# Kernel tuning notes

Measured on AMD Instinct MI355X. Metric: run time of the kernel, lower is better.

Reference implementation:

```python
import jax, jax.numpy as jnp
import numpy as np

N_NODES = 100000
N_EDGES = 1600000
IN_DIM, HIDDEN_DIM, OUT_DIM = 500, 64, 40


def setup_inputs() -> dict:
    key = jax.random.key(0)
    k1, k2, k3, k4, k5 = jax.random.split(key, 5)
    x = jax.random.normal(k1, (N_NODES, IN_DIM), dtype=jnp.float32)
    edge_index = jax.random.randint(k2, (2, N_EDGES), 0, N_NODES, dtype=jnp.int64)
    # Glorot-style init like PyG GCNConv
    W1 = jax.random.normal(k3, (IN_DIM, HIDDEN_DIM), dtype=jnp.float32) / np.sqrt(IN_DIM)
    b1 = jnp.zeros((HIDDEN_DIM,), dtype=jnp.float32)
    W2 = jax.random.normal(k4, (HIDDEN_DIM, OUT_DIM), dtype=jnp.float32) / np.sqrt(HIDDEN_DIM)
    b2 = jnp.zeros((OUT_DIM,), dtype=jnp.float32)
    return {"x": x, "W1": W1, "b1": b1, "W2": W2, "b2": b2, "edge_index": edge_index}


def _gcn_conv(x, W, b, src, dst, n):
    """PyG GCNConv: h = D^{-1/2} (A + I) D^{-1/2} (x W) + b."""
    h = x @ W  # transform first, propagate in smaller dim
    loops = jnp.arange(n, dtype=src.dtype)
    s = jnp.concatenate([src, loops])
    d = jnp.concatenate([dst, loops])
    deg = jax.ops.segment_sum(jnp.ones_like(d, dtype=h.dtype), d, num_segments=n)
    dinv = jnp.where(deg > 0, jax.lax.rsqrt(deg), 0.0)
    norm = dinv[s] * dinv[d]               # [E+N]
    msg = h[s] * norm[:, None]             # gather + scale
    out = jax.ops.segment_sum(msg, d, num_segments=n)  # scatter-add
    return out + b


def reference(x, W1, b1, W2, b2, edge_index):
    src, dst = edge_index[0], edge_index[1]
    n = x.shape[0]
    h = _gcn_conv(x, W1, b1, src, dst, n)
    h = jax.nn.relu(h)  # eval mode: dropout is identity
    out = _gcn_conv(h, W2, b2, src, dst, n)
    return out
```

## Files before the change

### kernel.cpp

```cpp
#include <hip/hip_runtime.h>
#include <cstdint>
#include <cstddef>

#define NN 100000
#define NE 1600000
#define IND 500
#define HD 64
#define OD 40
#define NBLK ((NN + 255) / 256)
#define KSTEPS 16
#define NTT 16
#define EB 1563

typedef __attribute__((ext_vector_type(8))) short short8v;
typedef __attribute__((ext_vector_type(8))) __bf16 bf16x8;
typedef __attribute__((ext_vector_type(4))) float float4v;

template <class V>
static __device__ __forceinline__ auto mfma_bf16_(V a, V b, float4v c, int)
    -> decltype(__builtin_amdgcn_mfma_f32_16x16x32_bf16(a, b, c, 0, 0, 0)) {
    return __builtin_amdgcn_mfma_f32_16x16x32_bf16(a, b, c, 0, 0, 0);
}
template <class V>
static __device__ __forceinline__ float4v mfma_bf16_(V a, V b, float4v c, long) {
    return __builtin_amdgcn_mfma_f32_16x16x32_bf16((bf16x8)a, (bf16x8)b, c, 0, 0, 0);
}
static __device__ __forceinline__ float4v mfma16(short8v a, short8v b, float4v c) {
    return mfma_bf16_(a, b, c, 0);
}

static __device__ __forceinline__ float bf2f(unsigned short v) {
    return __uint_as_float((unsigned)v << 16);
}
static __device__ __forceinline__ unsigned short f2bf(float v) {
    unsigned u = __float_as_uint(v);
    return (unsigned short)((u + 0x7fffu + ((u >> 16) & 1u)) >> 16);
}

typedef __attribute__((address_space(3))) char lds_char;
typedef const __attribute__((address_space(1))) char g_char;
static __device__ __forceinline__ void gl16(const char* g, char* l) {
    __builtin_amdgcn_global_load_lds((g_char*)g, (lds_char*)l, 16, 0, 0);
}

static __device__ __forceinline__ int detect64(const void* ei) {
    const unsigned* u = (const unsigned*)ei;
    int is64 = 1;
    #pragma unroll
    for (int i = 1; i < 16; i += 2)
        if (u[i] != 0u) is64 = 0;
    return is64;
}

static __device__ __forceinline__ void load4e(const void* ei, int is64, size_t base, int v[4]) {
    if (is64) {
        int4 a = ((const int4*)ei)[base >> 1];
        int4 b = ((const int4*)ei)[(base >> 1) + 1];
        v[0] = a.x; v[1] = a.z; v[2] = b.x; v[3] = b.z;
    } else {
        int4 a = *(const int4*)((const int*)ei + base);
        v[0] = a.x; v[1] = a.y; v[2] = a.z; v[3] = a.w;
    }
}

__global__ __launch_bounds__(256) void k_count_prep(const void* ei, int* cnt,
                                                    int* __restrict__ rank,
                                                    const float* __restrict__ W,
                                                    unsigned short* __restrict__ wh,
                                                    unsigned short* __restrict__ wl) {
    const int is64 = detect64(ei);
    int e0 = (blockIdx.x * 256 + threadIdx.x) * 4;
    if (e0 < NE) {
        int d[4];
        load4e(ei, is64, (size_t)NE + e0, d);
        int4 r;
        r.x = atomicAdd(&cnt[d[0]], 1);
        r.y = atomicAdd(&cnt[d[1]], 1);
        r.z = atomicAdd(&cnt[d[2]], 1);
        r.w = atomicAdd(&cnt[d[3]], 1);
        *(int4*)(rank + e0) = r;
    }
    int t = blockIdx.x * 256 + threadIdx.x;
    if (t < KSTEPS * 4 * 64) {
        int l = t & 63;
        int f = (t >> 6) & 3;
        int s = t >> 8;
        int n = f * 16 + (l & 15);
        int kbase = s * 32 + 8 * (l >> 4);
        unsigned short* ph = wh + (size_t)t * 8;
        unsigned short* pl = wl + (size_t)t * 8;
        #pragma unroll
        for (int j = 0; j < 8; ++j) {
            int k = kbase + j;
            float v = (k < IND) ? W[(size_t)k * HD + n] : 0.f;
            unsigned u = __float_as_uint(v);
            ph[j] = (unsigned short)(u >> 16);
            float r = v - __uint_as_float(u & 0xffff0000u);
            pl[j] = f2bf(r);
        }
    }
}

__global__ __launch_bounds__(256) void k_scan_block(const int* __restrict__ cnt,
                                                    int* __restrict__ rowptr,
                                                    int* __restrict__ bsum,
                                                    float* __restrict__ dinv) {
    int t = threadIdx.x;
    int i = blockIdx.x * 256 + t;
    int v = (i < NN) ? cnt[i] : 0;
    if (i < NN) dinv[i] = rsqrtf((float)v + 1.0f);
    int inc = v;
    #pragma unroll
    for (int off = 1; off < 64; off <<= 1) {
        int u = __shfl_up(inc, off);
        if ((t & 63) >= off) inc += u;
    }
    __shared__ int wsum[4];
    if ((t & 63) == 63) wsum[t >> 6] = inc;
    __syncthreads();
    if (t == 0) {
        int a = 0;
        #pragma unroll
        for (int w = 0; w < 4; ++w) { int b = wsum[w]; wsum[w] = a; a += b; }
        bsum[blockIdx.x] = a;
    }
    __syncthreads();
    if (i < NN) rowptr[i] = inc - v + wsum[t >> 6];
}

__global__ __launch_bounds__(512) void k_scan_bsum(int* bsum) {
    int t = threadIdx.x;
    int v = (t < NBLK) ? bsum[t] : 0;
    int inc = v;
    #pragma unroll
    for (int off = 1; off < 64; off <<= 1) {
        int u = __shfl_up(inc, off);
        if ((t & 63) >= off) inc += u;
    }
    __shared__ int wsum[8];
    if ((t & 63) == 63) wsum[t >> 6] = inc;
    __syncthreads();
    if (t == 0) {
        int a = 0;
        #pragma unroll
        for (int w = 0; w < 8; ++w) { int b = wsum[w]; wsum[w] = a; a += b; }
    }
    __syncthreads();
    if (t < NBLK) bsum[t] = inc - v + wsum[t >> 6];
}

__global__ void k_scan_add(int* rowptr, const int* __restrict__ bsum) {
    int i = blockIdx.x * 256 + threadIdx.x;
    if (i < NN) rowptr[i] += bsum[i >> 8];
    if (i == 0) rowptr[NN] = NE;
}

__global__ void k_scatter(const void* ei, const int* __restrict__ rowptr,
                          const int* __restrict__ rank, int* __restrict__ srcs) {
    int e0 = (blockIdx.x * 256 + threadIdx.x) * 4;
    if (e0 >= NE) return;
    const int is64 = detect64(ei);
    int s[4], d[4];
    load4e(ei, is64, (size_t)e0, s);
    load4e(ei, is64, (size_t)NE + e0, d);
    int4 r = *(const int4*)(rank + e0);
    srcs[rowptr[d[0]] + r.x] = s[0];
    srcs[rowptr[d[1]] + r.y] = s[1];
    srcs[rowptr[d[2]] + r.z] = s[2];
    srcs[rowptr[d[3]] + r.w] = s[3];
}

static __device__ __forceinline__ void split8f(float4 u0, float4 u1,
                                               short8v& hi, short8v& lo) {
    float t[8] = {u0.x, u0.y, u0.z, u0.w, u1.x, u1.y, u1.z, u1.w};
    #pragma unroll
    for (int j = 0; j < 8; ++j) {
        unsigned q = __float_as_uint(t[j]);
        hi[j] = (short)(q >> 16);
        float r = t[j] - __uint_as_float(q & 0xffff0000u);
        lo[j] = (short)f2bf(r);
    }
}

__global__ __launch_bounds__(256, 5) void k_gemm1m(const float* __restrict__ x,
                                                   const char* __restrict__ whb,
                                                   const char* __restrict__ wlb,
                                                   const float* __restrict__ dinv,
                                                   unsigned short* __restrict__ h) {
    __shared__ char smem[32768];
    const int tid  = threadIdx.x;
    const int lane = tid & 63;
    const int wave = tid >> 6;
    const int row0 = blockIdx.x * 64;
    const int rA = lane & 15;
    const int cg = lane >> 4;

    auto stage = [&](int kt, int buf) {
        const bool tail = (kt == NTT - 1);
        #pragma unroll
        for (int i = 0; i < 2; ++i) {
            int slot = i * 256 + tid;
            int r = slot >> 3, c = slot & 7;
            int cs = c ^ (r & 7);
            if (tail && cs > 4) cs = 4;
            int rsrc = row0 + r; if (rsrc >= NN) rsrc = NN - 1;
            const char* g = (const char*)x + (size_t)rsrc * (IND * 4) + kt * 128 + cs * 16;
            char* l = smem + buf * 16384 + (i * 256 + wave * 64) * 16;
            gl16(g, l);
        }
        #pragma unroll
        for (int i = 0; i < 2; ++i) {
            int j = i * 256 + tid;
            const char* src = (j < 256 ? whb : wlb) + kt * 4096 + (size_t)(j & 255) * 16;
            char* l = smem + buf * 16384 + 8192 + (i * 256 + wave * 64) * 16;
            gl16(src, l);
        }
    };

    float4v acc[4];
    const float4v zero4 = {0.f, 0.f, 0.f, 0.f};
    #pragma unroll
    for (int f = 0; f < 4; ++f) acc[f] = zero4;

    stage(0, 0);
    stage(1, 1);

    const int rbase = (wave * 16 + rA) * 8;
    const int sw = rA & 7;

    for (int kt = 0; kt < NTT; ++kt) {
        if (kt + 1 < NTT) asm volatile("s_waitcnt vmcnt(4)\ns_barrier" ::: "memory");
        else              asm volatile("s_waitcnt vmcnt(0)\ns_barrier" ::: "memory");
        const float4*  pa = (const float4*)(smem + (kt & 1) * 16384);
        const short8v* pb = (const short8v*)(smem + (kt & 1) * 16384 + 8192);
        int ch = cg * 2;
        float4 u0 = pa[rbase + (ch ^ sw)];
        float4 u1 = pa[rbase + ((ch + 1) ^ sw)];
        short8v ah, al;
        split8f(u0, u1, ah, al);
        #pragma unroll
        for (int f = 0; f < 4; ++f) {
            short8v vh = pb[f * 64 + lane];
            short8v vl = pb[256 + f * 64 + lane];
            acc[f] = mfma16(al, vh, acc[f]);
            acc[f] = mfma16(ah, vl, acc[f]);
            acc[f] = mfma16(ah, vh, acc[f]);
        }
        if (kt + 2 < NTT) {
            asm volatile("s_barrier" ::: "memory");
            stage(kt + 2, kt & 1);
        }
    }

    #pragma unroll
    for (int j = 0; j < 4; ++j) {
        int row = row0 + wave * 16 + cg * 4 + j;
        if (row < NN) {
            float dv = dinv[row];
            #pragma unroll
            for (int f = 0; f < 4; ++f)
                h[(size_t)row * HD + f * 16 + rA] = f2bf(acc[f][j] * dv);
        }
    }
}

__global__ __launch_bounds__(256) void k_agg1(const int* __restrict__ rowptr,
                                              const int* __restrict__ srcs,
                                              const float* __restrict__ dinv,
                                              const unsigned short* __restrict__ hb,
                                              const float* __restrict__ bias,
                                              unsigned short* __restrict__ outb) {
    int wid = (blockIdx.x * 256 + threadIdx.x) >> 6;
    int lane = threadIdx.x & 63;
    if (wid >= NN) return;
    float acc = bf2f(hb[(size_t)wid * HD + lane]);
    int beg = rowptr[wid];
    int cnt = rowptr[wid + 1] - beg;
    for (int base = 0; base < cnt; base += 64) {
        int m = cnt - base; if (m > 64) m = 64;
        int sj = (lane < m) ? srcs[beg + base + lane] : 0;
        int j = 0;
        for (; j + 8 <= m; j += 8) {
            int s0 = __builtin_amdgcn_readlane(sj, j);
            int s1 = __builtin_amdgcn_readlane(sj, j + 1);
            int s2 = __builtin_amdgcn_readlane(sj, j + 2);
            int s3 = __builtin_amdgcn_readlane(sj, j + 3);
            int s4 = __builtin_amdgcn_readlane(sj, j + 4);
            int s5 = __builtin_amdgcn_readlane(sj, j + 5);
            int s6 = __builtin_amdgcn_readlane(sj, j + 6);
            int s7 = __builtin_amdgcn_readlane(sj, j + 7);
            float v0 = bf2f(hb[(size_t)s0 * HD + lane]);
            float v1 = bf2f(hb[(size_t)s1 * HD + lane]);
            float v2 = bf2f(hb[(size_t)s2 * HD + lane]);
            float v3 = bf2f(hb[(size_t)s3 * HD + lane]);
            float v4 = bf2f(hb[(size_t)s4 * HD + lane]);
            float v5 = bf2f(hb[(size_t)s5 * HD + lane]);
            float v6 = bf2f(hb[(size_t)s6 * HD + lane]);
            float v7 = bf2f(hb[(size_t)s7 * HD + lane]);
            acc += ((v0 + v1) + (v2 + v3)) + ((v4 + v5) + (v6 + v7));
        }
        for (; j < m; ++j) {
            int s = __builtin_amdgcn_readlane(sj, j);
            acc += bf2f(hb[(size_t)s * HD + lane]);
        }
    }
    float dn = dinv[wid];
    outb[(size_t)wid * HD + lane] = f2bf(fmaxf(acc * dn + bias[lane], 0.f) * dn);
}

__global__ __launch_bounds__(256) void k_agg2_gemm2(const int* __restrict__ rowptr,
                                                    const int* __restrict__ srcs,
                                                    const float* __restrict__ dinv,
                                                    const unsigned short* __restrict__ hb,
                                                    const float* __restrict__ W2,
                                                    const float* __restrict__ b2,
                                                    float* __restrict__ out) {
    __shared__ float ws2[HD][OD];
    __shared__ float hsh[4][HD];
    const int t = threadIdx.x;
    for (int i = t; i < HD * OD; i += 256)
        ws2[i / OD][i % OD] = W2[i];

    int wid = (blockIdx.x * 256 + t) >> 6;
    int lane = t & 63;
    int w = t >> 6;
    float acc = bf2f(hb[(size_t)wid * HD + lane]);
    int beg = rowptr[wid];
    int cnt = rowptr[wid + 1] - beg;
    for (int base = 0; base < cnt; base += 64) {
        int m = cnt - base; if (m > 64) m = 64;
        int sj = (lane < m) ? srcs[beg + base + lane] : 0;
        int j = 0;
        for (; j + 8 <= m; j += 8) {
            int s0 = __builtin_amdgcn_readlane(sj, j);
            int s1 = __builtin_amdgcn_readlane(sj, j + 1);
            int s2 = __builtin_amdgcn_readlane(sj, j + 2);
            int s3 = __builtin_amdgcn_readlane(sj, j + 3);
            int s4 = __builtin_amdgcn_readlane(sj, j + 4);
            int s5 = __builtin_amdgcn_readlane(sj, j + 5);
            int s6 = __builtin_amdgcn_readlane(sj, j + 6);
            int s7 = __builtin_amdgcn_readlane(sj, j + 7);
            float v0 = bf2f(hb[(size_t)s0 * HD + lane]);
            float v1 = bf2f(hb[(size_t)s1 * HD + lane]);
            float v2 = bf2f(hb[(size_t)s2 * HD + lane]);
            float v3 = bf2f(hb[(size_t)s3 * HD + lane]);
            float v4 = bf2f(hb[(size_t)s4 * HD + lane]);
            float v5 = bf2f(hb[(size_t)s5 * HD + lane]);
            float v6 = bf2f(hb[(size_t)s6 * HD + lane]);
            float v7 = bf2f(hb[(size_t)s7 * HD + lane]);
            acc += ((v0 + v1) + (v2 + v3)) + ((v4 + v5) + (v6 + v7));
        }
        for (; j < m; ++j) {
            int s = __builtin_amdgcn_readlane(sj, j);
            acc += bf2f(hb[(size_t)s * HD + lane]);
        }
    }
    hsh[w][lane] = acc * dinv[wid];
    __syncthreads();
    if (lane < OD) {
        float s = b2[lane];
        #pragma unroll
        for (int k = 0; k < HD; ++k)
            s = fmaf(hsh[w][k], ws2[k][lane], s);
        out[(size_t)wid * OD + lane] = s;
    }
}

extern "C" void kernel_launch(void* const* d_in, const int* in_sizes, int n_in,
                              void* d_out, int out_size, void* d_ws, size_t ws_size,
                              hipStream_t stream) {
    const float* x  = (const float*)d_in[0];
    const float* W1 = (const float*)d_in[1];
    const float* b1 = (const float*)d_in[2];
    const float* W2 = (const float*)d_in[3];
    const float* b2 = (const float*)d_in[4];
    const void*  ei = d_in[5];
    float* out = (float*)d_out;

    char* ws = (char*)d_ws;
    unsigned short* h1b    = (unsigned short*)ws;
    unsigned short* hrelub = (unsigned short*)(ws + 12800000);
    int*   rowptr = (int*)(ws + 25600000);
    int*   cnt    = (int*)(ws + 26000896);
    int*   bsum   = (int*)(ws + 26401792);
    int*   srcs   = (int*)(ws + 26403840);
    int*   rank   = (int*)(ws + 32803840);
    float* dinv   = (float*)(ws + 39203840);
    unsigned short* wh = (unsigned short*)(ws + 39604224);
    unsigned short* wl = (unsigned short*)(ws + 39669760);

    hipMemsetAsync(cnt, 0, (size_t)NN * 4, stream);
    k_count_prep<<<EB, 256, 0, stream>>>(ei, cnt, rank, W1, wh, wl);
    k_scan_block<<<NBLK, 256, 0, stream>>>(cnt, rowptr, bsum, dinv);
    k_scan_bsum<<<1, 512, 0, stream>>>(bsum);
    k_scan_add<<<NBLK, 256, 0, stream>>>(rowptr, bsum);
    k_scatter<<<EB, 256, 0, stream>>>(ei, rowptr, rank, srcs);
    k_gemm1m<<<EB, 256, 0, stream>>>(x, (const char*)wh, (const char*)wl, dinv, h1b);
    k_agg1<<<(NN * 64) / 256, 256, 0, stream>>>(rowptr, srcs, dinv, h1b, b1, hrelub);
    k_agg2_gemm2<<<(NN * 64) / 256, 256, 0, stream>>>(rowptr, srcs, dinv, hrelub, W2, b2, out);
}
```

Measured before the change: 303.0 us.

## Fuse CSR scatter into GEMM1 kernel and unroll gather loop to 16

The edge scatter that builds the CSR source list is moved into the tail of the first GEMM kernel, which uses the same grid size, so one kernel launch and its dependency gap go away. The scatter's memory traffic can also overlap with GEMM work in other blocks. Separately, the neighbor gather in both aggregation kernels is factored into a helper that issues 16 independent loads per step instead of 8, for more memory-level parallelism. The wider unroll adds register pressure, and the GEMM kernel gains extra tail work.

```diff
diff --git a/kernel.cpp b/kernel.cpp
--- a/kernel.cpp
+++ b/kernel.cpp
@@ -155,21 +155,6 @@
     if (i == 0) rowptr[NN] = NE;
 }
 
-__global__ void k_scatter(const void* ei, const int* __restrict__ rowptr,
-                          const int* __restrict__ rank, int* __restrict__ srcs) {
-    int e0 = (blockIdx.x * 256 + threadIdx.x) * 4;
-    if (e0 >= NE) return;
-    const int is64 = detect64(ei);
-    int s[4], d[4];
-    load4e(ei, is64, (size_t)e0, s);
-    load4e(ei, is64, (size_t)NE + e0, d);
-    int4 r = *(const int4*)(rank + e0);
-    srcs[rowptr[d[0]] + r.x] = s[0];
-    srcs[rowptr[d[1]] + r.y] = s[1];
-    srcs[rowptr[d[2]] + r.z] = s[2];
-    srcs[rowptr[d[3]] + r.w] = s[3];
-}
-
 static __device__ __forceinline__ void split8f(float4 u0, float4 u1,
                                                short8v& hi, short8v& lo) {
     float t[8] = {u0.x, u0.y, u0.z, u0.w, u1.x, u1.y, u1.z, u1.w};
@@ -186,7 +171,11 @@
                                                    const char* __restrict__ whb,
                                                    const char* __restrict__ wlb,
                                                    const float* __restrict__ dinv,
-                                                   unsigned short* __restrict__ h) {
+                                                   unsigned short* __restrict__ h,
+                                                   const void* __restrict__ ei,
+                                                   const int* __restrict__ rowptr,
+                                                   const int* __restrict__ rank,
+                                                   int* __restrict__ srcs) {
     __shared__ char smem[32768];
     const int tid  = threadIdx.x;
     const int lane = tid & 63;
@@ -262,6 +251,60 @@
                 h[(size_t)row * HD + f * 16 + rA] = f2bf(acc[f][j] * dv);
         }
     }
+
+    {
+        int e0 = (blockIdx.x * 256 + tid) * 4;
+        if (e0 < NE) {
+            const int is64 = detect64(ei);
+            int s[4], d[4];
+            load4e(ei, is64, (size_t)e0, s);
+            load4e(ei, is64, (size_t)NE + e0, d);
+            int4 r = *(const int4*)(rank + e0);
+            srcs[rowptr[d[0]] + r.x] = s[0];
+            srcs[rowptr[d[1]] + r.y] = s[1];
+            srcs[rowptr[d[2]] + r.z] = s[2];
+            srcs[rowptr[d[3]] + r.w] = s[3];
+        }
+    }
+}
+
+static __device__ __forceinline__ float csr_gather(const int* __restrict__ rowptr,
+                                                   const int* __restrict__ srcs,
+                                                   const unsigned short* __restrict__ hb,
+                                                   int wid, int lane, float acc) {
+    int beg = rowptr[wid];
+    int cnt = rowptr[wid + 1] - beg;
+    for (int base = 0; base < cnt; base += 64) {
+        int m = cnt - base; if (m > 64) m = 64;
+        int sj = (lane < m) ? srcs[beg + base + lane] : 0;
+        int j = 0;
+        for (; j + 16 <= m; j += 16) {
+            float v[16];
+            #pragma unroll
+            for (int q = 0; q < 16; ++q) {
+                int sq = __builtin_amdgcn_readlane(sj, j + q);
+                v[q] = bf2f(hb[(size_t)sq * HD + lane]);
+            }
+            float t0 = ((v[0] + v[1]) + (v[2] + v[3])) + ((v[4] + v[5]) + (v[6] + v[7]));
+            float t1 = ((v[8] + v[9]) + (v[10] + v[11])) + ((v[12] + v[13]) + (v[14] + v[15]));
+            acc += t0 + t1;
+        }
+        if (j + 8 <= m) {
+            float v[8];
+            #pragma unroll
+            for (int q = 0; q < 8; ++q) {
+                int sq = __builtin_amdgcn_readlane(sj, j + q);
+                v[q] = bf2f(hb[(size_t)sq * HD + lane]);
+            }
+            acc += ((v[0] + v[1]) + (v[2] + v[3])) + ((v[4] + v[5]) + (v[6] + v[7]));
+            j += 8;
+        }
+        for (; j < m; ++j) {
+            int s = __builtin_amdgcn_readlane(sj, j);
+            acc += bf2f(hb[(size_t)s * HD + lane]);
+        }
+    }
+    return acc;
 }
 
 __global__ __launch_bounds__(256) void k_agg1(const int* __restrict__ rowptr,
@@ -274,36 +317,7 @@
     int lane = threadIdx.x & 63;
     if (wid >= NN) return;
     float acc = bf2f(hb[(size_t)wid * HD + lane]);
-    int beg = rowptr[wid];
-    int cnt = rowptr[wid + 1] - beg;
-    for (int base = 0; base < cnt; base += 64) {
-        int m = cnt - base; if (m > 64) m = 64;
-        int sj = (lane < m) ? srcs[beg + base + lane] : 0;
-        int j = 0;
-        for (; j + 8 <= m; j += 8) {
-            int s0 = __builtin_amdgcn_readlane(sj, j);
-            int s1 = __builtin_amdgcn_readlane(sj, j + 1);
-            int s2 = __builtin_amdgcn_readlane(sj, j + 2);
-            int s3 = __builtin_amdgcn_readlane(sj, j + 3);
-            int s4 = __builtin_amdgcn_readlane(sj, j + 4);
-            int s5 = __builtin_amdgcn_readlane(sj, j + 5);
-            int s6 = __builtin_amdgcn_readlane(sj, j + 6);
-            int s7 = __builtin_amdgcn_readlane(sj, j + 7);
-            float v0 = bf2f(hb[(size_t)s0 * HD + lane]);
-            float v1 = bf2f(hb[(size_t)s1 * HD + lane]);
-            float v2 = bf2f(hb[(size_t)s2 * HD + lane]);
-            float v3 = bf2f(hb[(size_t)s3 * HD + lane]);
-            float v4 = bf2f(hb[(size_t)s4 * HD + lane]);
-            float v5 = bf2f(hb[(size_t)s5 * HD + lane]);
-            float v6 = bf2f(hb[(size_t)s6 * HD + lane]);
-            float v7 = bf2f(hb[(size_t)s7 * HD + lane]);
-            acc += ((v0 + v1) + (v2 + v3)) + ((v4 + v5) + (v6 + v7));
-        }
-        for (; j < m; ++j) {
-            int s = __builtin_amdgcn_readlane(sj, j);
-            acc += bf2f(hb[(size_t)s * HD + lane]);
-        }
-    }
+    acc = csr_gather(rowptr, srcs, hb, wid, lane, acc);
     float dn = dinv[wid];
     outb[(size_t)wid * HD + lane] = f2bf(fmaxf(acc * dn + bias[lane], 0.f) * dn);
 }
@@ -325,36 +339,7 @@
     int lane = t & 63;
     int w = t >> 6;
     float acc = bf2f(hb[(size_t)wid * HD + lane]);
-    int beg = rowptr[wid];
-    int cnt = rowptr[wid + 1] - beg;
-    for (int base = 0; base < cnt; base += 64) {
-        int m = cnt - base; if (m > 64) m = 64;
-        int sj = (lane < m) ? srcs[beg + base + lane] : 0;
-        int j = 0;
-        for (; j + 8 <= m; j += 8) {
-            int s0 = __builtin_amdgcn_readlane(sj, j);
-            int s1 = __builtin_amdgcn_readlane(sj, j + 1);
-            int s2 = __builtin_amdgcn_readlane(sj, j + 2);
-            int s3 = __builtin_amdgcn_readlane(sj, j + 3);
-            int s4 = __builtin_amdgcn_readlane(sj, j + 4);
-            int s5 = __builtin_amdgcn_readlane(sj, j + 5);
-            int s6 = __builtin_amdgcn_readlane(sj, j + 6);
-            int s7 = __builtin_amdgcn_readlane(sj, j + 7);
-            float v0 = bf2f(hb[(size_t)s0 * HD + lane]);
-            float v1 = bf2f(hb[(size_t)s1 * HD + lane]);
-            float v2 = bf2f(hb[(size_t)s2 * HD + lane]);
-            float v3 = bf2f(hb[(size_t)s3 * HD + lane]);
-            float v4 = bf2f(hb[(size_t)s4 * HD + lane]);
-            float v5 = bf2f(hb[(size_t)s5 * HD + lane]);
-            float v6 = bf2f(hb[(size_t)s6 * HD + lane]);
-            float v7 = bf2f(hb[(size_t)s7 * HD + lane]);
-            acc += ((v0 + v1) + (v2 + v3)) + ((v4 + v5) + (v6 + v7));
-        }
-        for (; j < m; ++j) {
-            int s = __builtin_amdgcn_readlane(sj, j);
-            acc += bf2f(hb[(size_t)s * HD + lane]);
-        }
-    }
+    acc = csr_gather(rowptr, srcs, hb, wid, lane, acc);
     hsh[w][lane] = acc * dinv[wid];
     __syncthreads();
     if (lane < OD) {
@@ -394,8 +379,8 @@
     k_scan_block<<<NBLK, 256, 0, stream>>>(cnt, rowptr, bsum, dinv);
     k_scan_bsum<<<1, 512, 0, stream>>>(bsum);
     k_scan_add<<<NBLK, 256, 0, stream>>>(rowptr, bsum);
-    k_scatter<<<EB, 256, 0, stream>>>(ei, rowptr, rank, srcs);
-    k_gemm1m<<<EB, 256, 0, stream>>>(x, (const char*)wh, (const char*)wl, dinv, h1b);
+    k_gemm1m<<<EB, 256, 0, stream>>>(x, (const char*)wh, (const char*)wl, dinv, h1b,
+                                     ei, rowptr, rank, srcs);
     k_agg1<<<(NN * 64) / 256, 256, 0, stream>>>(rowptr, srcs, dinv, h1b, b1, hrelub);
     k_agg2_gemm2<<<(NN * 64) / 256, 256, 0, stream>>>(rowptr, srcs, dinv, hrelub, W2, b2, out);
 }
```

Measured after the change: 307.9 us. Within noise of the previous version (+1.6%).

## Project layer-2 features before aggregation using an MFMA projection kernel

Applied to the files above, without the earlier changes.

Reorders the second GCN layer so that the 64-to-40 weight transform runs first in a new MFMA kernel (k_proj), storing the projected features as bf16. Neighbour aggregation then gathers 40-wide rows instead of 64-wide ones. This also removes the per-block shared-memory load of W2 and the scalar per-node GEMM. In exchange there is one extra kernel launch and an extra 8MB write and read of the projected matrix. Lanes 40-63 still issue gathers whose results are thrown away.

```diff
diff --git a/kernel.cpp b/kernel.cpp
--- a/kernel.cpp
+++ b/kernel.cpp
@@ -65,9 +65,12 @@
 
 __global__ __launch_bounds__(256) void k_count_prep(const void* ei, int* cnt,
                                                     int* __restrict__ rank,
-                                                    const float* __restrict__ W,
+                                                    const float* __restrict__ W1,
                                                     unsigned short* __restrict__ wh,
-                                                    unsigned short* __restrict__ wl) {
+                                                    unsigned short* __restrict__ wl,
+                                                    const float* __restrict__ W2,
+                                                    unsigned short* __restrict__ wh2,
+                                                    unsigned short* __restrict__ wl2) {
     const int is64 = detect64(ei);
     int e0 = (blockIdx.x * 256 + threadIdx.x) * 4;
     if (e0 < NE) {
@@ -92,7 +95,26 @@
         #pragma unroll
         for (int j = 0; j < 8; ++j) {
             int k = kbase + j;
-            float v = (k < IND) ? W[(size_t)k * HD + n] : 0.f;
+            float v = (k < IND) ? W1[(size_t)k * HD + n] : 0.f;
+            unsigned u = __float_as_uint(v);
+            ph[j] = (unsigned short)(u >> 16);
+            float r = v - __uint_as_float(u & 0xffff0000u);
+            pl[j] = f2bf(r);
+        }
+    }
+    if (t >= 4096 && t < 4096 + 384) {
+        int t2 = t - 4096;
+        int l = t2 & 63;
+        int f = (t2 >> 6) % 3;
+        int s = t2 / 192;
+        int n = f * 16 + (l & 15);
+        int kbase = s * 32 + 8 * (l >> 4);
+        unsigned short* ph = wh2 + (size_t)t2 * 8;
+        unsigned short* pl = wl2 + (size_t)t2 * 8;
+        #pragma unroll
+        for (int j = 0; j < 8; ++j) {
+            int k = kbase + j;
+            float v = (n < OD) ? W2[(size_t)k * OD + n] : 0.f;
             unsigned u = __float_as_uint(v);
             ph[j] = (unsigned short)(u >> 16);
             float r = v - __uint_as_float(u & 0xffff0000u);
@@ -308,23 +330,54 @@
     outb[(size_t)wid * HD + lane] = f2bf(fmaxf(acc * dn + bias[lane], 0.f) * dn);
 }
 
-__global__ __launch_bounds__(256) void k_agg2_gemm2(const int* __restrict__ rowptr,
-                                                    const int* __restrict__ srcs,
-                                                    const float* __restrict__ dinv,
-                                                    const unsigned short* __restrict__ hb,
-                                                    const float* __restrict__ W2,
-                                                    const float* __restrict__ b2,
-                                                    float* __restrict__ out) {
-    __shared__ float ws2[HD][OD];
-    __shared__ float hsh[4][HD];
-    const int t = threadIdx.x;
-    for (int i = t; i < HD * OD; i += 256)
-        ws2[i / OD][i % OD] = W2[i];
-
-    int wid = (blockIdx.x * 256 + t) >> 6;
-    int lane = t & 63;
-    int w = t >> 6;
-    float acc = bf2f(hb[(size_t)wid * HD + lane]);
+__global__ __launch_bounds__(256) void k_proj(const unsigned short* __restrict__ hr,
+                                              const short8v* __restrict__ wh2,
+                                              const short8v* __restrict__ wl2,
+                                              unsigned short* __restrict__ p) {
+    const int lane = threadIdx.x & 63;
+    const int wave = threadIdx.x >> 6;
+    const int row0 = (blockIdx.x * 4 + wave) * 16;
+    if (row0 >= NN) return;
+    const int rA = lane & 15;
+    const int cg = lane >> 4;
+    float4v acc[3];
+    const float4v zero4 = {0.f, 0.f, 0.f, 0.f};
+    #pragma unroll
+    for (int f = 0; f < 3; ++f) acc[f] = zero4;
+    const unsigned short* ap = hr + (size_t)(row0 + rA) * HD + cg * 8;
+    #pragma unroll
+    for (int s = 0; s < 2; ++s) {
+        short8v a = *(const short8v*)(ap + s * 32);
+        #pragma unroll
+        for (int f = 0; f < 3; ++f) {
+            short8v vh = wh2[(s * 3 + f) * 64 + lane];
+            short8v vl = wl2[(s * 3 + f) * 64 + lane];
+            acc[f] = mfma16(a, vl, acc[f]);
+            acc[f] = mfma16(a, vh, acc[f]);
+        }
+    }
+    #pragma unroll
+    for (int j = 0; j < 4; ++j) {
+        int row = row0 + cg * 4 + j;
+        #pragma unroll
+        for (int f = 0; f < 3; ++f) {
+            int c = f * 16 + rA;
+            if (c < OD)
+                p[(size_t)row * OD + c] = f2bf(acc[f][j]);
+        }
+    }
+}
+
+__global__ __launch_bounds__(256) void k_agg2(const int* __restrict__ rowptr,
+                                              const int* __restrict__ srcs,
+                                              const float* __restrict__ dinv,
+                                              const unsigned short* __restrict__ pb,
+                                              const float* __restrict__ b2,
+                                              float* __restrict__ out) {
+    int wid = (blockIdx.x * 256 + threadIdx.x) >> 6;
+    int lane = threadIdx.x & 63;
+    if (wid >= NN) return;
+    float acc = bf2f(pb[(size_t)wid * OD + lane]);
     int beg = rowptr[wid];
     int cnt = rowptr[wid + 1] - beg;
     for (int base = 0; base < cnt; base += 64) {
@@ -340,30 +393,23 @@
             int s5 = __builtin_amdgcn_readlane(sj, j + 5);
             int s6 = __builtin_amdgcn_readlane(sj, j + 6);
             int s7 = __builtin_amdgcn_readlane(sj, j + 7);
-            float v0 = bf2f(hb[(size_t)s0 * HD + lane]);
-            float v1 = bf2f(hb[(size_t)s1 * HD + lane]);
-            float v2 = bf2f(hb[(size_t)s2 * HD + lane]);
-            float v3 = bf2f(hb[(size_t)s3 * HD + lane]);
-            float v4 = bf2f(hb[(size_t)s4 * HD + lane]);
-            float v5 = bf2f(hb[(size_t)s5 * HD + lane]);
-            float v6 = bf2f(hb[(size_t)s6 * HD + lane]);
-            float v7 = bf2f(hb[(size_t)s7 * HD + lane]);
+            float v0 = bf2f(pb[(size_t)s0 * OD + lane]);
+            float v1 = bf2f(pb[(size_t)s1 * OD + lane]);
+            float v2 = bf2f(pb[(size_t)s2 * OD + lane]);
+            float v3 = bf2f(pb[(size_t)s3 * OD + lane]);
+            float v4 = bf2f(pb[(size_t)s4 * OD + lane]);
+            float v5 = bf2f(pb[(size_t)s5 * OD + lane]);
+            float v6 = bf2f(pb[(size_t)s6 * OD + lane]);
+            float v7 = bf2f(pb[(size_t)s7 * OD + lane]);
             acc += ((v0 + v1) + (v2 + v3)) + ((v4 + v5) + (v6 + v7));
         }
         for (; j < m; ++j) {
             int s = __builtin_amdgcn_readlane(sj, j);
-            acc += bf2f(hb[(size_t)s * HD + lane]);
-        }
-    }
-    hsh[w][lane] = acc * dinv[wid];
-    __syncthreads();
-    if (lane < OD) {
-        float s = b2[lane];
-        #pragma unroll
-        for (int k = 0; k < HD; ++k)
-            s = fmaf(hsh[w][k], ws2[k][lane], s);
-        out[(size_t)wid * OD + lane] = s;
-    }
+            acc += bf2f(pb[(size_t)s * OD + lane]);
+        }
+    }
+    if (lane < OD)
+        out[(size_t)wid * OD + lane] = acc * dinv[wid] + b2[lane];
 }
 
 extern "C" void kernel_launch(void* const* d_in, const int* in_sizes, int n_in,
@@ -379,6 +425,7 @@
 
     char* ws = (char*)d_ws;
     unsigned short* h1b    = (unsigned short*)ws;
+    unsigned short* pb     = (unsigned short*)ws;
     unsigned short* hrelub = (unsigned short*)(ws + 12800000);
     int*   rowptr = (int*)(ws + 25600000);
     int*   cnt    = (int*)(ws + 26000896);
@@ -386,16 +433,19 @@
     int*   srcs   = (int*)(ws + 26403840);
     int*   rank   = (int*)(ws + 32803840);
     float* dinv   = (float*)(ws + 39203840);
-    unsigned short* wh = (unsigned short*)(ws + 39604224);
-    unsigned short* wl = (unsigned short*)(ws + 39669760);
+    unsigned short* wh  = (unsigned short*)(ws + 39604224);
+    unsigned short* wl  = (unsigned short*)(ws + 39669760);
+    unsigned short* wh2 = (unsigned short*)(ws + 39735296);
+    unsigned short* wl2 = (unsigned short*)(ws + 39741440);
 
     hipMemsetAsync(cnt, 0, (size_t)NN * 4, stream);
-    k_count_prep<<<EB, 256, 0, stream>>>(ei, cnt, rank, W1, wh, wl);
+    k_count_prep<<<EB, 256, 0, stream>>>(ei, cnt, rank, W1, wh, wl, W2, wh2, wl2);
     k_scan_block<<<NBLK, 256, 0, stream>>>(cnt, rowptr, bsum, dinv);
     k_scan_bsum<<<1, 512, 0, stream>>>(bsum);
     k_scan_add<<<NBLK, 256, 0, stream>>>(rowptr, bsum);
     k_scatter<<<EB, 256, 0, stream>>>(ei, rowptr, rank, srcs);
     k_gemm1m<<<EB, 256, 0, stream>>>(x, (const char*)wh, (const char*)wl, dinv, h1b);
     k_agg1<<<(NN * 64) / 256, 256, 0, stream>>>(rowptr, srcs, dinv, h1b, b1, hrelub);
-    k_agg2_gemm2<<<(NN * 64) / 256, 256, 0, stream>>>(rowptr, srcs, dinv, hrelub, W2, b2, out);
-}
+    k_proj<<<(NN / 16 + 3) / 4, 256, 0, stream>>>(hrelub, (const short8v*)wh2, (const short8v*)wl2, pb);
+    k_agg2<<<(NN * 64) / 256, 256, 0, stream>>>(rowptr, srcs, dinv, pb, b2, out);
+}
```

Result: faster. 267.7 us (-11.7%).

## Project to output dim before second aggregation and fold block-scan offsets into consumers

Applied to the files above, without the earlier changes.

The W2 projection moves into the first aggregation kernel. Each node's ReLU hidden vector is multiplied by W2 and stored as a 40-wide bf16 row, so the second aggregation gathers 40 features per edge instead of 64. The separate scan-add kernel is removed: consumers now add the per-block prefix sums to the block-local row pointers, and `rowptr[NN]` is written by the scan kernel. This cuts gather bandwidth in the second layer and one launch. In exchange, 24 of 64 lanes sit idle in the second gather, the 80-byte rows straddle cache lines, and every row-pointer lookup does an extra read.

```diff
diff --git a/kernel.cpp b/kernel.cpp
--- a/kernel.cpp
+++ b/kernel.cpp
@@ -65,7 +65,7 @@
 
 __global__ __launch_bounds__(256) void k_count_prep(const void* ei, int* cnt,
                                                     int* __restrict__ rank,
-                                                    const float* __restrict__ W,
+                                                    const float* __restrict__ W1,
                                                     unsigned short* __restrict__ wh,
                                                     unsigned short* __restrict__ wl) {
     const int is64 = detect64(ei);
@@ -92,7 +92,7 @@
         #pragma unroll
         for (int j = 0; j < 8; ++j) {
             int k = kbase + j;
-            float v = (k < IND) ? W[(size_t)k * HD + n] : 0.f;
+            float v = (k < IND) ? W1[(size_t)k * HD + n] : 0.f;
             unsigned u = __float_as_uint(v);
             ph[j] = (unsigned short)(u >> 16);
             float r = v - __uint_as_float(u & 0xffff0000u);
@@ -125,7 +125,7 @@
         bsum[blockIdx.x] = a;
     }
     __syncthreads();
-    if (i < NN) rowptr[i] = inc - v + wsum[t >> 6];
+    if (i <= NN) rowptr[i] = inc - v + wsum[t >> 6];
 }
 
 __global__ __launch_bounds__(512) void k_scan_bsum(int* bsum) {
@@ -149,13 +149,8 @@
     if (t < NBLK) bsum[t] = inc - v + wsum[t >> 6];
 }
 
-__global__ void k_scan_add(int* rowptr, const int* __restrict__ bsum) {
-    int i = blockIdx.x * 256 + threadIdx.x;
-    if (i < NN) rowptr[i] += bsum[i >> 8];
-    if (i == 0) rowptr[NN] = NE;
-}
-
-__global__ void k_scatter(const void* ei, const int* __restrict__ rowptr,
+__global__ void k_scatter(const void* ei, const int* __restrict__ rp,
+                          const int* __restrict__ bs,
                           const int* __restrict__ rank, int* __restrict__ srcs) {
     int e0 = (blockIdx.x * 256 + threadIdx.x) * 4;
     if (e0 >= NE) return;
@@ -164,10 +159,10 @@
     load4e(ei, is64, (size_t)e0, s);
     load4e(ei, is64, (size_t)NE + e0, d);
     int4 r = *(const int4*)(rank + e0);
-    srcs[rowptr[d[0]] + r.x] = s[0];
-    srcs[rowptr[d[1]] + r.y] = s[1];
-    srcs[rowptr[d[2]] + r.z] = s[2];
-    srcs[rowptr[d[3]] + r.w] = s[3];
+    srcs[rp[d[0]] + bs[d[0] >> 8] + r.x] = s[0];
+    srcs[rp[d[1]] + bs[d[1] >> 8] + r.y] = s[1];
+    srcs[rp[d[2]] + bs[d[2] >> 8] + r.z] = s[2];
+    srcs[rp[d[3]] + bs[d[3] >> 8] + r.w] = s[3];
 }
 
 static __device__ __forceinline__ void split8f(float4 u0, float4 u1,
@@ -264,18 +259,26 @@
     }
 }
 
-__global__ __launch_bounds__(256) void k_agg1(const int* __restrict__ rowptr,
-                                              const int* __restrict__ srcs,
-                                              const float* __restrict__ dinv,
-                                              const unsigned short* __restrict__ hb,
-                                              const float* __restrict__ bias,
-                                              unsigned short* __restrict__ outb) {
-    int wid = (blockIdx.x * 256 + threadIdx.x) >> 6;
-    int lane = threadIdx.x & 63;
-    if (wid >= NN) return;
+__global__ __launch_bounds__(256) void k_agg1proj(const int* __restrict__ rp,
+                                                  const int* __restrict__ bs,
+                                                  const int* __restrict__ srcs,
+                                                  const float* __restrict__ dinv,
+                                                  const unsigned short* __restrict__ hb,
+                                                  const float* __restrict__ bias,
+                                                  const float* __restrict__ W2,
+                                                  unsigned short* __restrict__ pb) {
+    __shared__ float ws2[HD][OD];
+    __shared__ float hsh[4][HD];
+    const int t = threadIdx.x;
+    for (int i = t; i < HD * OD; i += 256)
+        ws2[i / OD][i % OD] = W2[i];
+
+    int wid = (blockIdx.x * 256 + t) >> 6;
+    int lane = t & 63;
+    int w = t >> 6;
     float acc = bf2f(hb[(size_t)wid * HD + lane]);
-    int beg = rowptr[wid];
-    int cnt = rowptr[wid + 1] - beg;
+    int beg = rp[wid] + bs[wid >> 8];
+    int cnt = rp[wid + 1] + bs[(wid + 1) >> 8] - beg;
     for (int base = 0; base < cnt; base += 64) {
         int m = cnt - base; if (m > 64) m = 64;
         int sj = (lane < m) ? srcs[beg + base + lane] : 0;
@@ -305,28 +308,30 @@
         }
     }
     float dn = dinv[wid];
-    outb[(size_t)wid * HD + lane] = f2bf(fmaxf(acc * dn + bias[lane], 0.f) * dn);
-}
-
-__global__ __launch_bounds__(256) void k_agg2_gemm2(const int* __restrict__ rowptr,
-                                                    const int* __restrict__ srcs,
-                                                    const float* __restrict__ dinv,
-                                                    const unsigned short* __restrict__ hb,
-                                                    const float* __restrict__ W2,
-                                                    const float* __restrict__ b2,
-                                                    float* __restrict__ out) {
-    __shared__ float ws2[HD][OD];
-    __shared__ float hsh[4][HD];
-    const int t = threadIdx.x;
-    for (int i = t; i < HD * OD; i += 256)
-        ws2[i / OD][i % OD] = W2[i];
-
-    int wid = (blockIdx.x * 256 + t) >> 6;
-    int lane = t & 63;
-    int w = t >> 6;
-    float acc = bf2f(hb[(size_t)wid * HD + lane]);
-    int beg = rowptr[wid];
-    int cnt = rowptr[wid + 1] - beg;
+    hsh[w][lane] = fmaxf(acc * dn + bias[lane], 0.f) * dn;
+    __syncthreads();
+    if (lane < OD) {
+        float s = 0.f;
+        #pragma unroll
+        for (int k = 0; k < HD; ++k)
+            s = fmaf(hsh[w][k], ws2[k][lane], s);
+        pb[(size_t)wid * OD + lane] = f2bf(s);
+    }
+}
+
+__global__ __launch_bounds__(256) void k_agg2(const int* __restrict__ rp,
+                                              const int* __restrict__ bs,
+                                              const int* __restrict__ srcs,
+                                              const float* __restrict__ dinv,
+                                              const unsigned short* __restrict__ pb,
+                                              const float* __restrict__ b2,
+                                              float* __restrict__ out) {
+    int wid = (blockIdx.x * 256 + threadIdx.x) >> 6;
+    int lane = threadIdx.x & 63;
+    if (wid >= NN) return;
+    float acc = bf2f(pb[(size_t)wid * OD + lane]);
+    int beg = rp[wid] + bs[wid >> 8];
+    int cnt = rp[wid + 1] + bs[(wid + 1) >> 8] - beg;
     for (int base = 0; base < cnt; base += 64) {
         int m = cnt - base; if (m > 64) m = 64;
         int sj = (lane < m) ? srcs[beg + base + lane] : 0;
@@ -340,30 +345,23 @@
             int s5 = __builtin_amdgcn_readlane(sj, j + 5);
             int s6 = __builtin_amdgcn_readlane(sj, j + 6);
             int s7 = __builtin_amdgcn_readlane(sj, j + 7);
-            float v0 = bf2f(hb[(size_t)s0 * HD + lane]);
-            float v1 = bf2f(hb[(size_t)s1 * HD + lane]);
-            float v2 = bf2f(hb[(size_t)s2 * HD + lane]);
-            float v3 = bf2f(hb[(size_t)s3 * HD + lane]);
-            float v4 = bf2f(hb[(size_t)s4 * HD + lane]);
-            float v5 = bf2f(hb[(size_t)s5 * HD + lane]);
-            float v6 = bf2f(hb[(size_t)s6 * HD + lane]);
-            float v7 = bf2f(hb[(size_t)s7 * HD + lane]);
+            float v0 = bf2f(pb[(size_t)s0 * OD + lane]);
+            float v1 = bf2f(pb[(size_t)s1 * OD + lane]);
+            float v2 = bf2f(pb[(size_t)s2 * OD + lane]);
+            float v3 = bf2f(pb[(size_t)s3 * OD + lane]);
+            float v4 = bf2f(pb[(size_t)s4 * OD + lane]);
+            float v5 = bf2f(pb[(size_t)s5 * OD + lane]);
+            float v6 = bf2f(pb[(size_t)s6 * OD + lane]);
+            float v7 = bf2f(pb[(size_t)s7 * OD + lane]);
             acc += ((v0 + v1) + (v2 + v3)) + ((v4 + v5) + (v6 + v7));
         }
         for (; j < m; ++j) {
             int s = __builtin_amdgcn_readlane(sj, j);
-            acc += bf2f(hb[(size_t)s * HD + lane]);
-        }
-    }
-    hsh[w][lane] = acc * dinv[wid];
-    __syncthreads();
-    if (lane < OD) {
-        float s = b2[lane];
-        #pragma unroll
-        for (int k = 0; k < HD; ++k)
-            s = fmaf(hsh[w][k], ws2[k][lane], s);
-        out[(size_t)wid * OD + lane] = s;
-    }
+            acc += bf2f(pb[(size_t)s * OD + lane]);
+        }
+    }
+    if (lane < OD)
+        out[(size_t)wid * OD + lane] = acc * dinv[wid] + b2[lane];
 }
 
 extern "C" void kernel_launch(void* const* d_in, const int* in_sizes, int n_in,
@@ -378,24 +376,23 @@
     float* out = (float*)d_out;
 
     char* ws = (char*)d_ws;
-    unsigned short* h1b    = (unsigned short*)ws;
-    unsigned short* hrelub = (unsigned short*)(ws + 12800000);
+    unsigned short* h1b   = (unsigned short*)ws;
+    unsigned short* pb    = (unsigned short*)(ws + 12800000);
     int*   rowptr = (int*)(ws + 25600000);
     int*   cnt    = (int*)(ws + 26000896);
     int*   bsum   = (int*)(ws + 26401792);
     int*   srcs   = (int*)(ws + 26403840);
     int*   rank   = (int*)(ws + 32803840);
     float* dinv   = (float*)(ws + 39203840);
-    unsigned short* wh = (unsigned short*)(ws + 39604224);
-    unsigned short* wl = (unsigned short*)(ws + 39669760);
+    unsigned short* wh  = (unsigned short*)(ws + 39604224);
+    unsigned short* wl  = (unsigned short*)(ws + 39669760);
 
     hipMemsetAsync(cnt, 0, (size_t)NN * 4, stream);
     k_count_prep<<<EB, 256, 0, stream>>>(ei, cnt, rank, W1, wh, wl);
     k_scan_block<<<NBLK, 256, 0, stream>>>(cnt, rowptr, bsum, dinv);
     k_scan_bsum<<<1, 512, 0, stream>>>(bsum);
-    k_scan_add<<<NBLK, 256, 0, stream>>>(rowptr, bsum);
-    k_scatter<<<EB, 256, 0, stream>>>(ei, rowptr, rank, srcs);
+    k_scatter<<<EB, 256, 0, stream>>>(ei, rowptr, bsum, rank, srcs);
     k_gemm1m<<<EB, 256, 0, stream>>>(x, (const char*)wh, (const char*)wl, dinv, h1b);
-    k_agg1<<<(NN * 64) / 256, 256, 0, stream>>>(rowptr, srcs, dinv, h1b, b1, hrelub);
-    k_agg2_gemm2<<<(NN * 64) / 256, 256, 0, stream>>>(rowptr, srcs, dinv, hrelub, W2, b2, out);
-}
+    k_agg1proj<<<(NN * 64) / 256, 256, 0, stream>>>(rowptr, bsum, srcs, dinv, h1b, b1, W2, pb);
+    k_agg2<<<(NN * 64) / 256, 256, 0, stream>>>(rowptr, bsum, srcs, dinv, pb, b2, out);
+}
```

Result: faster. 291.9 us (-3.7%).
